# Optimization experiments

Measured on AMD Instinct MI355X. Metric: run time of the kernel, lower is better.

Reference implementation:

```python
import jax, jax.numpy as jnp
import numpy as np

ETA = 0.01   # Hebbian learning rate of the plasticity rule
LR = 1.0     # CircuitModel.lr


def setup_inputs() -> dict:
    key = jax.random.key(0)
    k1, k2, k3 = jax.random.split(key, 3)
    B, T, NI, NO, NOBS = 64, 256, 512, 512, 128
    X = jax.random.normal(k1, (B, T, NI), dtype=jnp.float32)
    W_init = jax.random.normal(k2, (B, NO, NI), dtype=jnp.float32) * 0.1
    observed_idx = jnp.sort(jax.random.randint(k3, (NOBS,), 0, NO))
    return {"X": X, "W_init": W_init, "observed_idx": observed_idx}


def reference(X, W_init, observed_idx):
    # X: [B,T,NI], W_init: [B,NO,NI], observed_idx: [NOBS] int
    NO = W_init.shape[1]
    mask = jnp.zeros((NO,), X.dtype).at[observed_idx].set(1.0)  # [NO]

    def step(W, x_t):
        # x_t: [B,NI]
        pre = jnp.einsum('boi,bi->bo', W, x_t)          # [B,NO]
        y = jax.nn.sigmoid(pre)
        m = y[:, observed_idx]                           # [B,NOBS] recorded before masking
        y_sparse = y * mask                              # zero unobserved outputs
        W = W * mask[None, :, None]                      # zero unobserved rows of W
        dW = ETA * (y_sparse[:, :, None] * x_t[:, None, :])  # Hebbian outer product
        return W + LR * dW, m

    _, m_traj = jax.lax.scan(step, W_init, jnp.swapaxes(X, 0, 1))  # [T,B,NOBS]
    return jnp.swapaxes(m_traj, 0, 1)  # [B,T,NOBS]
```

## Files before the change

### kernel.cpp

```cpp
#include <hip/hip_runtime.h>

#define NB   64
#define NT   256
#define NI   512
#define NO   512
#define NOBS 128
#define ETA  0.01f

typedef __attribute__((ext_vector_type(8))) short bf16x8;
typedef __attribute__((ext_vector_type(4))) float f32x4;

__device__ __forceinline__ unsigned short f2bf(float f) {
    unsigned int u = __float_as_uint(f);
    return (unsigned short)((u + 0x7fffu + ((u >> 16) & 1u)) >> 16);
}

__device__ __forceinline__ unsigned cvtpk(float lo, float hi) {
    unsigned r;
    asm("v_cvt_pk_bf16_f32 %0, %1, %2" : "=v"(r) : "v"(lo), "v"(hi));
    return r;
}

__global__ __launch_bounds__(256)
void k1_gemm(const float* __restrict__ Xf, const float* __restrict__ Wf,
             const int* __restrict__ obs,
             float* __restrict__ Gd, unsigned short* __restrict__ Gh,
             float* __restrict__ P0)
{
    __shared__ unsigned short As[128 * 64];
    __shared__ unsigned short Bs[128 * 64];
    __shared__ int obsS[128];

    const int tid  = threadIdx.x;
    const int lane = tid & 63;
    const int wv   = tid >> 6;
    const int l16  = lane & 15;
    const int quad = lane >> 4;

    const int b   = blockIdx.x & 63;
    const int sub = blockIdx.x >> 6;

    if (tid < 128) obsS[tid] = obs[tid];
    __syncthreads();

    int bm = 0, bn = 0;
    if (sub < 3) {
        bm = (sub >= 1) ? 1 : 0;
        bn = (sub == 2) ? 1 : 0;
    } else {
        bm = sub - 3;
    }

    const int mrow = tid >> 3;
    const int ccol = tid & 7;
    const float* aP[4];
    const float* bP[4];
    int slotv[4];
#pragma unroll
    for (int it = 0; it < 4; ++it) {
        const int m = it * 32 + mrow;
        slotv[it] = m * 64 + ((ccol ^ (m & 7)) * 8);
        aP[it] = Xf + ((size_t)b * NT + bm * 128 + m) * NI + ccol * 8;
        bP[it] = (sub < 3)
                   ? Xf + ((size_t)b * NT + bn * 128 + m) * NI + ccol * 8
                   : Wf + ((size_t)b * NO + obsS[m]) * NI + ccol * 8;
    }

    const int wm = (wv >> 1) * 64;
    const int wn = (wv & 1) * 64;

    f32x4 acc[4][4] = {};

    for (int kb = 0; kb < NI / 64; ++kb) {
        __syncthreads();
#pragma unroll
        for (int it = 0; it < 4; ++it) {
            const float4 a0 = *(const float4*)(aP[it]);
            const float4 a1 = *(const float4*)(aP[it] + 4);
            const float4 b0 = *(const float4*)(bP[it]);
            const float4 b1 = *(const float4*)(bP[it] + 4);
            uint4 ap, bp;
            ap.x = cvtpk(a0.x, a0.y); ap.y = cvtpk(a0.z, a0.w);
            ap.z = cvtpk(a1.x, a1.y); ap.w = cvtpk(a1.z, a1.w);
            bp.x = cvtpk(b0.x, b0.y); bp.y = cvtpk(b0.z, b0.w);
            bp.z = cvtpk(b1.x, b1.y); bp.w = cvtpk(b1.z, b1.w);
            *(uint4*)&As[slotv[it]] = ap;
            *(uint4*)&Bs[slotv[it]] = bp;
            aP[it] += 64;
            bP[it] += 64;
        }
        __syncthreads();
#pragma unroll
        for (int ks = 0; ks < 2; ++ks) {
            const int q = ks * 4 + quad;
            bf16x8 af[4], bfr[4];
#pragma unroll
            for (int mt = 0; mt < 4; ++mt) {
                const int m = wm + mt * 16 + l16;
                af[mt] = *(const bf16x8*)&As[m * 64 + ((q ^ (m & 7)) * 8)];
            }
#pragma unroll
            for (int nt = 0; nt < 4; ++nt) {
                const int n = wn + nt * 16 + l16;
                bfr[nt] = *(const bf16x8*)&Bs[n * 64 + ((q ^ (n & 7)) * 8)];
            }
#pragma unroll
            for (int mt = 0; mt < 4; ++mt)
#pragma unroll
                for (int nt = 0; nt < 4; ++nt)
                    acc[mt][nt] = __builtin_amdgcn_mfma_f32_16x16x32_bf16(
                        af[mt], bfr[nt], acc[mt][nt], 0, 0, 0);
        }
    }

    if (sub < 3) {
        unsigned short* GhB = Gh + ((size_t)b << 16);
        float* GdB = Gd + ((size_t)b << 12);
#pragma unroll
        for (int mt = 0; mt < 4; ++mt)
#pragma unroll
            for (int nt = 0; nt < 4; ++nt) {
                const int gcol = bn * 128 + wn + nt * 16 + l16;
#pragma unroll
                for (int r = 0; r < 4; ++r) {
                    const int grow = bm * 128 + wm + mt * 16 + quad * 4 + r;
                    const float v = ETA * acc[mt][nt][r];
                    GhB[(size_t)grow * 256 + gcol] = f2bf(v);
                    if ((grow >> 4) == (gcol >> 4))
                        GdB[((grow >> 4) << 8) + ((grow & 15) << 4) + (gcol & 15)] = v;
                }
            }
    } else {
        float* Pb = P0 + (size_t)b * NT * NOBS + (size_t)bm * 128 * NOBS;
#pragma unroll
        for (int mt = 0; mt < 4; ++mt)
#pragma unroll
            for (int nt = 0; nt < 4; ++nt)
#pragma unroll
                for (int r = 0; r < 4; ++r)
                    Pb[(size_t)(wm + mt * 16 + quad * 4 + r) * NOBS
                       + wn + nt * 16 + l16] = acc[mt][nt][r];
    }
}


#define LDROW(Q0, Q1, Q2, Q3, U1)                                          \
    {                                                                      \
        if ((U1) <= 14) {                                                  \
            if ((U1) <= 2)  Q0 = *(const f32x4*)(gdc + (U1) * 16);         \
            if ((U1) <= 6)  Q1 = *(const f32x4*)(gdc + (U1) * 16 + 4);     \
            if ((U1) <= 10) Q2 = *(const f32x4*)(gdc + (U1) * 16 + 8);     \
            Q3 = *(const f32x4*)(gdc + (U1) * 16 + 12);                    \
        }                                                                  \
    }

#define GV(Q0, Q1, Q2, Q3, V)                                              \
    ((V) < 4 ? (Q0)[(V) & 3] : (V) < 8 ? (Q1)[(V) & 3]                     \
             : (V) < 12 ? (Q2)[(V) & 3] : (Q3)[(V) & 3])

#define SCAN_STEP(U, C0, C1, C2, C3, N0, N1, N2, N3)                       \
    {                                                                      \
        LDROW(N0, N1, N2, N3, (U) + 2)                                     \
        const float y = __builtin_amdgcn_rcpf(1.f + __expf(-p[(U)]));      \
        ob[obOff + (size_t)((U) * NOBS)] = y;                              \
        _Pragma("unroll")                                                  \
        for (int v = (U) + 1; v < 16; ++v)                                 \
            p[v] = fmaf(y, GV(C0, C1, C2, C3, v), p[v]);                   \
        if ((U) & 1)                                                       \
            ybf2[cp * 128 + ((U) >> 1) * 16 + j] =                         \
                (unsigned)f2bf(eprev) | ((unsigned)f2bf(y) << 16);         \
        else                                                               \
            eprev = y;                                                     \
    }

__global__ __launch_bounds__(512, 4)
void k2_scan(const float* __restrict__ Gd, const unsigned short* __restrict__ Gh,
             const float* __restrict__ P0, float* __restrict__ out)
{
    __shared__ float gdiag[16 * 16 * 16];
    __shared__ float preS[16 * 17];
    __shared__ unsigned int ybf2[2 * 8 * 16];

    const int tid  = threadIdx.x;
    const int lane = tid & 63;
    const int l16  = lane & 15;
    const int quad = lane >> 4;
    const int w    = __builtin_amdgcn_readfirstlane(tid >> 6);

    const int b  = blockIdx.x & 63;
    const int jg = blockIdx.x >> 6;

    const float* Pb = P0 + (size_t)b * NT * NOBS + jg * 16;
    const unsigned short* GhB = Gh + ((size_t)b << 16);
    float* ob = out + (size_t)b * NT * NOBS + jg * 16;

    {
        const f32x4* gs = (const f32x4*)(Gd + ((size_t)b << 12));
        ((f32x4*)gdiag)[tid]       = gs[tid];
        ((f32x4*)gdiag)[512 + tid] = gs[512 + tid];
    }

    f32x4 acc[2];
#pragma unroll
    for (int s2 = 0; s2 < 2; ++s2)
#pragma unroll
        for (int r = 0; r < 4; ++r)
            acc[s2][r] = Pb[(size_t)(w * 32 + s2 * 16 + quad * 4 + r) * NOBS + l16];

    const int T0 = 2 * w, T1 = 2 * w + 1;

    union AB { bf16x8 v; unsigned int d[4]; };
    AB Acur0, Acur1, Anext0, Anext1;
#pragma unroll
    for (int p2 = 0; p2 < 4; ++p2) {
        Acur0.d[p2] = 0; Acur1.d[p2] = 0; Anext0.d[p2] = 0; Anext1.d[p2] = 0;
    }
    if (quad < 2) {
        if (T0 > 0)
            Acur0.v = *(const bf16x8*)(GhB + (size_t)(T0 * 16 + l16) * 256 + quad * 8);
        Acur1.v = *(const bf16x8*)(GhB + (size_t)(T1 * 16 + l16) * 256 + quad * 8);
    }

    auto scan_chunk = [&](const int c, const f32x4 a) {
#pragma unroll
        for (int r = 0; r < 4; ++r)
            preS[(quad * 4 + r) * 17 + l16] = a[r];
        asm volatile("s_waitcnt lgkmcnt(0)" ::: "memory");
        __builtin_amdgcn_s_setprio(1);
        if (lane < 16) {
            const int j = lane;
            const int cp = c & 1;
            const float* gdc = gdiag + (c << 8);
            const size_t obOff = (size_t)(c << 4) * NOBS + j;
            float p[16];
#pragma unroll
            for (int u = 0; u < 16; ++u) p[u] = preS[u * 17 + j];
            f32x4 Aq0, Aq1, Aq2, Aq3, Bq0, Bq1, Bq2, Bq3, Cq0, Cq1, Cq2, Cq3;
            LDROW(Aq0, Aq1, Aq2, Aq3, 0)
            LDROW(Bq0, Bq1, Bq2, Bq3, 1)
            float eprev = 0.f;
            SCAN_STEP(0,  Aq0, Aq1, Aq2, Aq3, Cq0, Cq1, Cq2, Cq3)
            SCAN_STEP(1,  Bq0, Bq1, Bq2, Bq3, Aq0, Aq1, Aq2, Aq3)
            SCAN_STEP(2,  Cq0, Cq1, Cq2, Cq3, Bq0, Bq1, Bq2, Bq3)
            SCAN_STEP(3,  Aq0, Aq1, Aq2, Aq3, Cq0, Cq1, Cq2, Cq3)
            SCAN_STEP(4,  Bq0, Bq1, Bq2, Bq3, Aq0, Aq1, Aq2, Aq3)
            SCAN_STEP(5,  Cq0, Cq1, Cq2, Cq3, Bq0, Bq1, Bq2, Bq3)
            SCAN_STEP(6,  Aq0, Aq1, Aq2, Aq3, Cq0, Cq1, Cq2, Cq3)
            SCAN_STEP(7,  Bq0, Bq1, Bq2, Bq3, Aq0, Aq1, Aq2, Aq3)
            SCAN_STEP(8,  Cq0, Cq1, Cq2, Cq3, Bq0, Bq1, Bq2, Bq3)
            SCAN_STEP(9,  Aq0, Aq1, Aq2, Aq3, Cq0, Cq1, Cq2, Cq3)
            SCAN_STEP(10, Bq0, Bq1, Bq2, Bq3, Aq0, Aq1, Aq2, Aq3)
            SCAN_STEP(11, Cq0, Cq1, Cq2, Cq3, Bq0, Bq1, Bq2, Bq3)
            SCAN_STEP(12, Aq0, Aq1, Aq2, Aq3, Cq0, Cq1, Cq2, Cq3)
            SCAN_STEP(13, Bq0, Bq1, Bq2, Bq3, Aq0, Aq1, Aq2, Aq3)
            SCAN_STEP(14, Cq0, Cq1, Cq2, Cq3, Bq0, Bq1, Bq2, Bq3)
            SCAN_STEP(15, Aq0, Aq1, Aq2, Aq3, Cq0, Cq1, Cq2, Cq3)
        }
        __builtin_amdgcn_s_setprio(0);
    };

    if (w == 0)
        scan_chunk(0, acc[0]);
    __syncthreads();

#pragma unroll 1
    for (int c = 0; c < 15; ++c) {
        if (T1 > c) {
            AB B;
#pragma unroll
            for (int p2 = 0; p2 < 4; ++p2) B.d[p2] = 0;
            if (quad < 2) {
#pragma unroll
                for (int p2 = 0; p2 < 4; ++p2)
                    B.d[p2] = ybf2[(c & 1) * 128 + (quad * 4 + p2) * 16 + l16];
            }
#pragma unroll
            for (int p2 = 0; p2 < 4; ++p2) { Anext0.d[p2] = 0; Anext1.d[p2] = 0; }
            if (quad < 2) {
                if (T0 > c + 1)
                    Anext0.v = *(const bf16x8*)(GhB + (size_t)(T0 * 16 + l16) * 256
                                                + (c + 1) * 16 + quad * 8);
                if (T1 > c + 1)
                    Anext1.v = *(const bf16x8*)(GhB + (size_t)(T1 * 16 + l16) * 256
                                                + (c + 1) * 16 + quad * 8);
            }
            if (T0 > c)
                acc[0] = __builtin_amdgcn_mfma_f32_16x16x32_bf16(
                    Acur0.v, B.v, acc[0], 0, 0, 0);
            acc[1] = __builtin_amdgcn_mfma_f32_16x16x32_bf16(
                Acur1.v, B.v, acc[1], 0, 0, 0);
            if (w == ((c + 1) >> 1)) {
                if ((c + 1) & 1) scan_chunk(c + 1, acc[1]);
                else             scan_chunk(c + 1, acc[0]);
            }
            Acur0 = Anext0;
            Acur1 = Anext1;
        }
        __syncthreads();
    }
}

extern "C" void kernel_launch(void* const* d_in, const int* in_sizes, int n_in,
                              void* d_out, int out_size, void* d_ws, size_t ws_size,
                              hipStream_t stream)
{
    const float* X   = (const float*)d_in[0];
    const float* Wi  = (const float*)d_in[1];
    const int*   obs = (const int*)d_in[2];
    float*       out = (float*)d_out;

    float*          Gd = (float*)d_ws;
    float*          P0 = (float*)((char*)d_ws + (1u << 20));
    unsigned short* Gh = (unsigned short*)((char*)d_ws + (9u << 20));

    hipLaunchKernelGGL(k1_gemm, dim3(NB * 5), dim3(256), 0, stream,
                       X, Wi, obs, Gd, Gh, P0);
    hipLaunchKernelGGL(k2_scan, dim3(NB * 8), dim3(512), 0, stream,
                       Gd, Gh, P0, out);
}
```

Before: 147.7 us.

## Prefetch next K-tile into registers and skip duplicate B load on diagonal blocks

Restructures the k1_gemm main loop as a register double buffer: global loads for the next 64-wide K slice are issued before the MFMA work on the current slice, which is meant to hide global load latency behind compute. Diagonal Gram blocks (sub 0 and 2), where A and B are the same rows of X, now load and convert only A and read B fragments from the A shared tile. This halves global traffic for those blocks. The cost is roughly double the staging registers, which may lower occupancy.

```diff
diff --git a/kernel.cpp b/kernel.cpp
--- a/kernel.cpp
+++ b/kernel.cpp
@@ -20,6 +20,64 @@
     asm("v_cvt_pk_bf16_f32 %0, %1, %2" : "=v"(r) : "v"(lo), "v"(hi));
     return r;
 }
+
+
+#define K1_STEP(CA0, CA1, CB0, CB1, NA0, NA1, NB0, NB1, KB)                 \
+    {                                                                       \
+        __syncthreads();                                                    \
+        _Pragma("unroll")                                                   \
+        for (int it = 0; it < 4; ++it) {                                    \
+            uint4 ap;                                                       \
+            ap.x = cvtpk(CA0[it].x, CA0[it].y);                             \
+            ap.y = cvtpk(CA0[it].z, CA0[it].w);                             \
+            ap.z = cvtpk(CA1[it].x, CA1[it].y);                             \
+            ap.w = cvtpk(CA1[it].z, CA1[it].w);                             \
+            *(uint4*)&As[slotv[it]] = ap;                                   \
+            if (!sameAB) {                                                  \
+                uint4 bp;                                                   \
+                bp.x = cvtpk(CB0[it].x, CB0[it].y);                         \
+                bp.y = cvtpk(CB0[it].z, CB0[it].w);                         \
+                bp.z = cvtpk(CB1[it].x, CB1[it].y);                         \
+                bp.w = cvtpk(CB1[it].z, CB1[it].w);                         \
+                *(uint4*)&Bs[slotv[it]] = bp;                               \
+            }                                                               \
+        }                                                                   \
+        if ((KB) < 7) {       \
+            _Pragma("unroll")                                               \
+            for (int it = 0; it < 4; ++it) {                                \
+                NA0[it] = *(const float4*)(aP[it]);                         \
+                NA1[it] = *(const float4*)(aP[it] + 4);                     \
+                if (!sameAB) {                                              \
+                    NB0[it] = *(const float4*)(bP[it]);                     \
+                    NB1[it] = *(const float4*)(bP[it] + 4);                 \
+                }                                                           \
+                aP[it] += 64; bP[it] += 64;                                 \
+            }                                                               \
+        }                                                                   \
+        __syncthreads();                                                    \
+        const unsigned short* Bsrc = sameAB ? As : Bs;                      \
+        _Pragma("unroll")                                                   \
+        for (int ks = 0; ks < 2; ++ks) {                                    \
+            const int q = ks * 4 + quad;                                    \
+            bf16x8 af[4], bfr[4];                                           \
+            _Pragma("unroll")                                               \
+            for (int mt = 0; mt < 4; ++mt) {                                \
+                const int m = wm + mt * 16 + l16;                           \
+                af[mt] = *(const bf16x8*)&As[m * 64 + ((q ^ (m & 7)) * 8)]; \
+            }                                                               \
+            _Pragma("unroll")                                               \
+            for (int nt = 0; nt < 4; ++nt) {                                \
+                const int n = wn + nt * 16 + l16;                           \
+                bfr[nt] = *(const bf16x8*)&Bsrc[n * 64 + ((q ^ (n & 7)) * 8)];\
+            }                                                               \
+            _Pragma("unroll")                                               \
+            for (int mt = 0; mt < 4; ++mt)                                  \
+                _Pragma("unroll")                                           \
+                for (int nt = 0; nt < 4; ++nt)                              \
+                    acc[mt][nt] = __builtin_amdgcn_mfma_f32_16x16x32_bf16(  \
+                        af[mt], bfr[nt], acc[mt][nt], 0, 0, 0);             \
+        }                                                                   \
+    }
 
 __global__ __launch_bounds__(256)
 void k1_gemm(const float* __restrict__ Xf, const float* __restrict__ Wf,
@@ -50,6 +108,7 @@
     } else {
         bm = sub - 3;
     }
+    const bool sameAB = (sub == 0) || (sub == 2);
 
     const int mrow = tid >> 3;
     const int ccol = tid & 7;
@@ -71,46 +130,24 @@
 
     f32x4 acc[4][4] = {};
 
-    for (int kb = 0; kb < NI / 64; ++kb) {
-        __syncthreads();
-#pragma unroll
-        for (int it = 0; it < 4; ++it) {
-            const float4 a0 = *(const float4*)(aP[it]);
-            const float4 a1 = *(const float4*)(aP[it] + 4);
-            const float4 b0 = *(const float4*)(bP[it]);
-            const float4 b1 = *(const float4*)(bP[it] + 4);
-            uint4 ap, bp;
-            ap.x = cvtpk(a0.x, a0.y); ap.y = cvtpk(a0.z, a0.w);
-            ap.z = cvtpk(a1.x, a1.y); ap.w = cvtpk(a1.z, a1.w);
-            bp.x = cvtpk(b0.x, b0.y); bp.y = cvtpk(b0.z, b0.w);
-            bp.z = cvtpk(b1.x, b1.y); bp.w = cvtpk(b1.z, b1.w);
-            *(uint4*)&As[slotv[it]] = ap;
-            *(uint4*)&Bs[slotv[it]] = bp;
-            aP[it] += 64;
-            bP[it] += 64;
+    float4 cA0[4], cA1[4], cB0[4], cB1[4];
+    float4 nA0[4], nA1[4], nB0[4], nB1[4];
+
+#pragma unroll
+    for (int it = 0; it < 4; ++it) {
+        cA0[it] = *(const float4*)(aP[it]);
+        cA1[it] = *(const float4*)(aP[it] + 4);
+        if (!sameAB) {
+            cB0[it] = *(const float4*)(bP[it]);
+            cB1[it] = *(const float4*)(bP[it] + 4);
         }
-        __syncthreads();
-#pragma unroll
-        for (int ks = 0; ks < 2; ++ks) {
-            const int q = ks * 4 + quad;
-            bf16x8 af[4], bfr[4];
-#pragma unroll
-            for (int mt = 0; mt < 4; ++mt) {
-                const int m = wm + mt * 16 + l16;
-                af[mt] = *(const bf16x8*)&As[m * 64 + ((q ^ (m & 7)) * 8)];
-            }
-#pragma unroll
-            for (int nt = 0; nt < 4; ++nt) {
-                const int n = wn + nt * 16 + l16;
-                bfr[nt] = *(const bf16x8*)&Bs[n * 64 + ((q ^ (n & 7)) * 8)];
-            }
-#pragma unroll
-            for (int mt = 0; mt < 4; ++mt)
-#pragma unroll
-                for (int nt = 0; nt < 4; ++nt)
-                    acc[mt][nt] = __builtin_amdgcn_mfma_f32_16x16x32_bf16(
-                        af[mt], bfr[nt], acc[mt][nt], 0, 0, 0);
-        }
+        aP[it] += 64; bP[it] += 64;
+    }
+
+#pragma unroll 1
+    for (int kb2 = 0; kb2 < 4; ++kb2) {
+        K1_STEP(cA0, cA1, cB0, cB1, nA0, nA1, nB0, nB1, 2 * kb2)
+        K1_STEP(nA0, nA1, nB0, nB1, cA0, cA1, cB0, cB1, 2 * kb2 + 1)
     }
 
     if (sub < 3) {
```

After: 152.1 us. 3.0% more time.

## Merge Gram and projection tiles into four blocks per batch sharing the X tile

Applied to the files above, without the earlier changes.

The first kernel now launches four blocks per batch instead of five. Block 0 computes both the diagonal X·Xᵀ tile (using the A tile as its own B operand) and the first projection tile against the gathered W rows. This reuses the loaded X tile and removes one block's worth of global loads and conversions. In exchange that block does twice the MFMA work and holds two accumulator sets, which raises register pressure (launch bounds set to one block) and could make it the critical path.

```diff
diff --git a/kernel.cpp b/kernel.cpp
--- a/kernel.cpp
+++ b/kernel.cpp
@@ -21,7 +21,7 @@
     return r;
 }
 
-__global__ __launch_bounds__(256)
+__global__ __launch_bounds__(256, 1)
 void k1_gemm(const float* __restrict__ Xf, const float* __restrict__ Wf,
              const int* __restrict__ obs,
              float* __restrict__ Gd, unsigned short* __restrict__ Gh,
@@ -43,13 +43,12 @@
     if (tid < 128) obsS[tid] = obs[tid];
     __syncthreads();
 
-    int bm = 0, bn = 0;
-    if (sub < 3) {
-        bm = (sub >= 1) ? 1 : 0;
-        bn = (sub == 2) ? 1 : 0;
-    } else {
-        bm = sub - 3;
-    }
+    const bool doG = (sub <= 2);
+    const bool doP = (sub == 0) || (sub == 3);
+    const int  bm  = (sub >= 1) ? 1 : 0;
+    const int  bn  = (sub == 2) ? 1 : 0;
+    const int  pb  = (sub == 3) ? 1 : 0;
+    const bool bw  = !doG || (sub == 0);
 
     const int mrow = tid >> 3;
     const int ccol = tid & 7;
@@ -61,15 +60,17 @@
         const int m = it * 32 + mrow;
         slotv[it] = m * 64 + ((ccol ^ (m & 7)) * 8);
         aP[it] = Xf + ((size_t)b * NT + bm * 128 + m) * NI + ccol * 8;
-        bP[it] = (sub < 3)
-                   ? Xf + ((size_t)b * NT + bn * 128 + m) * NI + ccol * 8
-                   : Wf + ((size_t)b * NO + obsS[m]) * NI + ccol * 8;
+        bP[it] = bw
+                   ? Wf + ((size_t)b * NO + obsS[m]) * NI + ccol * 8
+                   : Xf + ((size_t)b * NT + ((sub == 2) ? 128 : 0) + m) * NI
+                       + ccol * 8;
     }
 
     const int wm = (wv >> 1) * 64;
     const int wn = (wv & 1) * 64;
 
-    f32x4 acc[4][4] = {};
+    f32x4 accG[4][4] = {};
+    f32x4 accP[4][4] = {};
 
     for (int kb = 0; kb < NI / 64; ++kb) {
         __syncthreads();
@@ -90,30 +91,48 @@
             bP[it] += 64;
         }
         __syncthreads();
+        const unsigned short* BsrcG = (sub == 0) ? As : Bs;
 #pragma unroll
         for (int ks = 0; ks < 2; ++ks) {
             const int q = ks * 4 + quad;
-            bf16x8 af[4], bfr[4];
+            bf16x8 af[4];
 #pragma unroll
             for (int mt = 0; mt < 4; ++mt) {
                 const int m = wm + mt * 16 + l16;
                 af[mt] = *(const bf16x8*)&As[m * 64 + ((q ^ (m & 7)) * 8)];
             }
-#pragma unroll
-            for (int nt = 0; nt < 4; ++nt) {
-                const int n = wn + nt * 16 + l16;
-                bfr[nt] = *(const bf16x8*)&Bs[n * 64 + ((q ^ (n & 7)) * 8)];
-            }
-#pragma unroll
-            for (int mt = 0; mt < 4; ++mt)
-#pragma unroll
-                for (int nt = 0; nt < 4; ++nt)
-                    acc[mt][nt] = __builtin_amdgcn_mfma_f32_16x16x32_bf16(
-                        af[mt], bfr[nt], acc[mt][nt], 0, 0, 0);
+            if (doG) {
+                bf16x8 bfr[4];
+#pragma unroll
+                for (int nt = 0; nt < 4; ++nt) {
+                    const int n = wn + nt * 16 + l16;
+                    bfr[nt] = *(const bf16x8*)&BsrcG[n * 64 + ((q ^ (n & 7)) * 8)];
+                }
+#pragma unroll
+                for (int mt = 0; mt < 4; ++mt)
+#pragma unroll
+                    for (int nt = 0; nt < 4; ++nt)
+                        accG[mt][nt] = __builtin_amdgcn_mfma_f32_16x16x32_bf16(
+                            af[mt], bfr[nt], accG[mt][nt], 0, 0, 0);
+            }
+            if (doP) {
+                bf16x8 bfr[4];
+#pragma unroll
+                for (int nt = 0; nt < 4; ++nt) {
+                    const int n = wn + nt * 16 + l16;
+                    bfr[nt] = *(const bf16x8*)&Bs[n * 64 + ((q ^ (n & 7)) * 8)];
+                }
+#pragma unroll
+                for (int mt = 0; mt < 4; ++mt)
+#pragma unroll
+                    for (int nt = 0; nt < 4; ++nt)
+                        accP[mt][nt] = __builtin_amdgcn_mfma_f32_16x16x32_bf16(
+                            af[mt], bfr[nt], accP[mt][nt], 0, 0, 0);
+            }
         }
     }
 
-    if (sub < 3) {
+    if (doG) {
         unsigned short* GhB = Gh + ((size_t)b << 16);
         float* GdB = Gd + ((size_t)b << 12);
 #pragma unroll
@@ -124,14 +143,15 @@
 #pragma unroll
                 for (int r = 0; r < 4; ++r) {
                     const int grow = bm * 128 + wm + mt * 16 + quad * 4 + r;
-                    const float v = ETA * acc[mt][nt][r];
+                    const float v = ETA * accG[mt][nt][r];
                     GhB[(size_t)grow * 256 + gcol] = f2bf(v);
                     if ((grow >> 4) == (gcol >> 4))
                         GdB[((grow >> 4) << 8) + ((grow & 15) << 4) + (gcol & 15)] = v;
                 }
             }
-    } else {
-        float* Pb = P0 + (size_t)b * NT * NOBS + (size_t)bm * 128 * NOBS;
+    }
+    if (doP) {
+        float* Pb = P0 + (size_t)b * NT * NOBS + (size_t)pb * 128 * NOBS;
 #pragma unroll
         for (int mt = 0; mt < 4; ++mt)
 #pragma unroll
@@ -139,7 +159,7 @@
 #pragma unroll
                 for (int r = 0; r < 4; ++r)
                     Pb[(size_t)(wm + mt * 16 + quad * 4 + r) * NOBS
-                       + wn + nt * 16 + l16] = acc[mt][nt][r];
+                       + wn + nt * 16 + l16] = accP[mt][nt][r];
     }
 }
 
@@ -313,7 +333,7 @@
     float*          P0 = (float*)((char*)d_ws + (1u << 20));
     unsigned short* Gh = (unsigned short*)((char*)d_ws + (9u << 20));
 
-    hipLaunchKernelGGL(k1_gemm, dim3(NB * 5), dim3(256), 0, stream,
+    hipLaunchKernelGGL(k1_gemm, dim3(NB * 4), dim3(256), 0, stream,
                        X, Wi, obs, Gd, Gh, P0);
     hipLaunchKernelGGL(k2_scan, dim3(NB * 8), dim3(512), 0, stream,
                        Gd, Gh, P0, out);
```

Measured after the change: 157.4 us. 6.5% more time.
